# Kernel optimization log

Measured on AMD Instinct MI355X. Metric: run time of the kernel, lower is better.

The kernel has to match this reference:

```python
import jax, jax.numpy as jnp
import numpy as np

EMBED_DIM = 384

def setup_inputs() -> dict:
    key = jax.random.key(0)
    k1, k2, k3 = jax.random.split(key, 3)
    B, P, N, d = 8, 4, 4096, EMBED_DIM
    hidden_states = jax.random.normal(k1, (B, P, N, d), dtype=jnp.float32)
    # 1x1 conv == pointwise linear over channel dim; scale like fan-in init
    w_qkv = jax.random.normal(k2, (d, 1 + 2 * d), dtype=jnp.float32) * (1.0 / np.sqrt(d))
    b_qkv = jnp.zeros((1 + 2 * d,), dtype=jnp.float32)
    w_out = jax.random.normal(k3, (d, d), dtype=jnp.float32) * (1.0 / np.sqrt(d))
    b_out = jnp.zeros((d,), dtype=jnp.float32)
    return {"hidden_states": hidden_states, "w_qkv": w_qkv, "b_qkv": b_qkv,
            "w_out": w_out, "b_out": b_out}

def reference(hidden_states, w_qkv, b_qkv, w_out, b_out):
    d = EMBED_DIM
    # qkv 1x1 conv (channels-last): [B,P,N,d] @ [d, 1+2d]
    qkv = jnp.einsum("bpnd,de->bpne", hidden_states, w_qkv) + b_qkv
    query = qkv[..., :1]                # [B,P,N,1]
    key_ = qkv[..., 1:1 + d]            # [B,P,N,d]
    value = qkv[..., 1 + d:]            # [B,P,N,d]
    # softmax over token axis (axis=2); attn_dropout=0.0 -> identity
    context_scores = jax.nn.softmax(query, axis=2)
    # softmax-weighted pooling of keys over tokens -> [B,P,1,d]
    context_vector = jnp.sum(key_ * context_scores, axis=2, keepdims=True)
    # relu-gated broadcast multiply
    out = context_vector * jax.nn.relu(value)
    # out 1x1 conv
    out = jnp.einsum("bpnd,de->bpne", out, w_out) + b_out
    return out
```

## Files before the change

kernel.cpp:

```cpp
#include <hip/hip_runtime.h>

#define D     384
#define E     769
#define NTOK  4096
#define BPN   32
#define NCH   64

typedef short s16x8 __attribute__((ext_vector_type(8)));
typedef float f32x4 __attribute__((ext_vector_type(4)));
typedef float f32x2 __attribute__((ext_vector_type(2)));

__device__ __forceinline__ unsigned short f2bf(float f){
  unsigned int u = __builtin_bit_cast(unsigned int, f);
  u += 0x7FFFu + ((u >> 16) & 1u);
  return (unsigned short)(u >> 16);
}

__global__ void k0_prep(const float* __restrict__ wqkv, const float* __restrict__ wout,
                        float* __restrict__ wq, unsigned short* __restrict__ wvF,
                        unsigned short* __restrict__ woF){
  int tid = blockIdx.x*256 + threadIdx.x;
  if (tid < D) wq[tid] = wqkv[(size_t)tid*E];
  if (tid < 24*12*64*8){
    int pos = tid & 7;
    int lane = (tid >> 3) & 63;
    int kt  = (tid >> 9) % 12;
    int nt  = tid / 6144;
    int l15 = lane & 15, l4 = lane >> 4;
    int col = nt*16 + l15;
    int k   = kt*32 + l4*8 + pos;
    wvF[tid] = f2bf(wqkv[(size_t)k*E + 385 + col]);
    woF[tid] = f2bf(wout[(size_t)k*D + col]);
  }
}

__global__ __launch_bounds__(384)
void kA_fused(const float* __restrict__ H, const float* __restrict__ wq,
              float* __restrict__ partial, float* __restrict__ mArr,
              float* __restrict__ lArr){
  __shared__ float Hs[32][D];
  __shared__ float qs[32];
  const int ch = blockIdx.x, bp = blockIdx.y;
  const int t = threadIdx.x;
  const int wave = t >> 6, lane = t & 63;

  f32x2 wqr[3];
  #pragma unroll
  for (int seg=0;seg<3;++seg)
    wqr[seg] = *reinterpret_cast<const f32x2*>(wq + lane*2 + seg*128);

  float acc = 0.f, mRun = -3.4e38f, lRun = 0.f;

  for (int s = 0; s < 2; ++s){
    if (s) __syncthreads();
    const size_t base = (size_t)bp*NTOK + (size_t)ch*64 + s*32;

    f32x2 h[6][3];
    #pragma unroll
    for (int j=0;j<6;++j){
      int r = wave + j*6;
      if (r < 32){
        const float* hr = H + (base + r)*D + lane*2;
        #pragma unroll
        for (int seg=0;seg<3;++seg)
          h[j][seg] = *reinterpret_cast<const f32x2*>(hr + seg*128);
      }
    }
    #pragma unroll
    for (int j=0;j<6;++j){
      int r = wave + j*6;
      if (r < 32){
        float a = 0.f;
        #pragma unroll
        for (int seg=0;seg<3;++seg){
          *reinterpret_cast<f32x2*>(&Hs[r][lane*2 + seg*128]) = h[j][seg];
          a += h[j][seg].x*wqr[seg].x + h[j][seg].y*wqr[seg].y;
        }
        #pragma unroll
        for (int off=32; off; off>>=1) a += __shfl_xor(a, off, 64);
        if (lane == 0) qs[r] = a;
      }
    }
    __syncthreads();

    float msub = qs[0];
    #pragma unroll
    for (int n=1;n<32;++n) msub = fmaxf(msub, qs[n]);
    float mNew  = fmaxf(mRun, msub);
    float scale = __expf(mRun - mNew);
    acc  *= scale;
    lRun *= scale;
    float lsub = 0.f;
    #pragma unroll 8
    for (int n=0;n<32;++n){
      float w = __expf(qs[n] - mNew);
      lsub += w;
      acc  += w * Hs[n][t];
    }
    lRun += lsub;
    mRun  = mNew;
  }

  partial[((size_t)bp*NCH + ch)*D + t] = acc;
  if (t == 0){ mArr[bp*NCH + ch] = mRun; lArr[bp*NCH + ch] = lRun; }
}

__global__ void kB_cv(const float* __restrict__ partial, const float* __restrict__ mArr,
                      const float* __restrict__ lArr, const float* __restrict__ wqkv,
                      const float* __restrict__ bqkv, float* __restrict__ cv){
  __shared__ float S[D];
  const int bp = blockIdx.x, t = threadIdx.x;
  float M = -3.4e38f;
  #pragma unroll 4
  for (int c = 0; c < NCH; ++c) M = fmaxf(M, mArr[bp*NCH + c]);
  float num = 0.f, den = 0.f;
  #pragma unroll 2
  for (int c = 0; c < NCH; ++c){
    float f = __expf(mArr[bp*NCH + c] - M);
    num += f * partial[((size_t)bp*NCH + c)*D + t];
    den += f * lArr[bp*NCH + c];
  }
  S[t] = num / den;
  __syncthreads();
  float acc = bqkv[1 + t];
  #pragma unroll 4
  for (int k = 0; k < D; ++k)
    acc += S[k] * wqkv[(size_t)k*E + 1 + t];
  cv[(size_t)bp*D + t] = acc;
}

#define BM 64
#define LOADW(W, kt, n) (*reinterpret_cast<const s16x8*>(&(W)[((size_t)((n)*12+(kt))*64 + lane)*8]))

__global__ __launch_bounds__(512, 2)
void k5_main(const float* __restrict__ H, const unsigned short* __restrict__ wvF,
             const unsigned short* __restrict__ woF, const float* __restrict__ cv,
             const float* __restrict__ bqkv, const float* __restrict__ bout,
             float* __restrict__ out){
  __shared__ unsigned short As[BM*D];
  const int bp = blockIdx.y;
  const int m0 = blockIdx.x*BM;
  const size_t rowbase = (size_t)bp*NTOK + m0;
  const float* A = H + rowbase*D;
  const int t = threadIdx.x;
  const int wave = t>>6, lane = t&63;
  const int l15 = lane&15, l4 = lane>>4;
  const int n0 = wave*48;
  const unsigned short* wvW = wvF + (size_t)wave*3*12*512;
  const unsigned short* woW = woF + (size_t)wave*3*12*512;

  #pragma unroll
  for (int i=0;i<12;++i){
    int c = t + i*512;
    int idx8 = c >> 1;
    int l15v = idx8 & 15;
    int l4v  = (idx8 >> 4) & 3;
    int ktv  = (idx8 >> 6) % 12;
    int mv   = idx8 / 768;
    f32x4 v = *reinterpret_cast<const f32x4*>(
        A + (size_t)(mv*16 + l15v)*D + ktv*32 + l4v*8 + (c&1)*4);
    ushort4 b;
    b.x=f2bf(v.x); b.y=f2bf(v.y); b.z=f2bf(v.z); b.w=f2bf(v.w);
    *reinterpret_cast<ushort4*>(&As[c*4]) = b;
  }

  s16x8 b0[3], b1[3];
  #pragma unroll
  for (int n=0;n<3;++n) b0[n] = LOADW(wvW, 0, n);
  #pragma unroll
  for (int n=0;n<3;++n) b1[n] = LOADW(wvW, 1, n);
  __syncthreads();

  f32x4 acc[4][3] = {};
  #pragma unroll
  for (int kt=0; kt<12; ++kt){
    s16x8 bp_[3];
    if (kt < 10){
      #pragma unroll
      for (int n=0;n<3;++n) bp_[n] = LOADW(wvW, kt+2, n);
    }
    s16x8 a[4];
    #pragma unroll
    for (int m=0;m<4;++m)
      a[m] = *reinterpret_cast<const s16x8*>(&As[((m*12+kt)*64 + lane)*8]);
    #pragma unroll
    for (int m=0;m<4;++m)
      #pragma unroll
      for (int n=0;n<3;++n)
        acc[m][n] = __builtin_amdgcn_mfma_f32_16x16x32_bf16(a[m], b0[n], acc[m][n], 0,0,0);
    #pragma unroll
    for (int n=0;n<3;++n){ b0[n] = b1[n]; b1[n] = bp_[n]; }
  }
  __syncthreads();

  float bv[3], cvv[3];
  #pragma unroll
  for (int n=0;n<3;++n){
    int col = n0 + n*16 + l15;
    bv[n]  = bqkv[385+col];
    cvv[n] = cv[(size_t)bp*D + col];
  }

  #pragma unroll
  for (int n=0;n<3;++n){
    int col  = n0 + n*16 + l15;
    int kt2  = col >> 5;
    int l42  = (col >> 3) & 3;
    int pos2 = col & 7;
    #pragma unroll
    for (int m=0;m<4;++m){
      #pragma unroll
      for (int r=0;r<4;++r){
        int row = l4*4 + r;
        float v = acc[m][n][r] + bv[n];
        v = v > 0.f ? v*cvv[n] : 0.f;
        As[((m*12+kt2)*64 + l42*16 + row)*8 + pos2] = f2bf(v);
      }
    }
  }
  #pragma unroll
  for (int m=0;m<4;++m)
    #pragma unroll
    for (int n=0;n<3;++n)
      acc[m][n] = (f32x4){0.f,0.f,0.f,0.f};

  #pragma unroll
  for (int n=0;n<3;++n) b0[n] = LOADW(woW, 0, n);
  #pragma unroll
  for (int n=0;n<3;++n) b1[n] = LOADW(woW, 1, n);
  __syncthreads();

  #pragma unroll
  for (int kt=0; kt<12; ++kt){
    s16x8 bp_[3];
    if (kt < 10){
      #pragma unroll
      for (int n=0;n<3;++n) bp_[n] = LOADW(woW, kt+2, n);
    }
    s16x8 a[4];
    #pragma unroll
    for (int m=0;m<4;++m)
      a[m] = *reinterpret_cast<const s16x8*>(&As[((m*12+kt)*64 + lane)*8]);
    #pragma unroll
    for (int m=0;m<4;++m)
      #pragma unroll
      for (int n=0;n<3;++n)
        acc[m][n] = __builtin_amdgcn_mfma_f32_16x16x32_bf16(a[m], b0[n], acc[m][n], 0,0,0);
    #pragma unroll
    for (int n=0;n<3;++n){ b0[n] = b1[n]; b1[n] = bp_[n]; }
  }

  #pragma unroll
  for (int n=0;n<3;++n){
    int col = n0 + n*16 + l15;
    float bo = bout[col];
    #pragma unroll
    for (int m=0;m<4;++m)
      #pragma unroll
      for (int r=0;r<4;++r){
        int row = m*16 + l4*4 + r;
        out[(rowbase+row)*D + col] = acc[m][n][r] + bo;
      }
  }
}

extern "C" void kernel_launch(void* const* d_in, const int* in_sizes, int n_in,
                              void* d_out, int out_size, void* d_ws, size_t ws_size,
                              hipStream_t stream){
  const float* H    = (const float*)d_in[0];
  const float* wqkv = (const float*)d_in[1];
  const float* bqkv = (const float*)d_in[2];
  const float* wout = (const float*)d_in[3];
  const float* bout = (const float*)d_in[4];
  float* out = (float*)d_out;

  char* ws = (char*)d_ws;
  float*          partial = (float*)(ws + 0x000000);
  float*          mArr    = (float*)(ws + 0x300000);
  float*          lArr    = (float*)(ws + 0x302000);
  float*          cv      = (float*)(ws + 0x304000);
  float*          wq      = (float*)(ws + 0x310000);
  unsigned short* wvF     = (unsigned short*)(ws + 0x311000);
  unsigned short* woF     = (unsigned short*)(ws + 0x359000);

  hipLaunchKernelGGL(k0_prep,  dim3(576),          dim3(256), 0, stream, wqkv, wout, wq, wvF, woF);
  hipLaunchKernelGGL(kA_fused, dim3(NCH, BPN),     dim3(384), 0, stream, H, wq, partial, mArr, lArr);
  hipLaunchKernelGGL(kB_cv,    dim3(BPN),          dim3(384), 0, stream, partial, mArr, lArr, wqkv, bqkv, cv);
  hipLaunchKernelGGL(k5_main,  dim3(NTOK/BM, BPN), dim3(512), 0, stream, H, wvF, woF, cv, bqkv, bout, out);
}
```

Baseline: 227.1 us.

## Prefetch second token chunk during pooling and compute softmax weights once per block

The fused pooling kernel now issues the global loads for the second 32-token chunk before it pools the first chunk, so that memory latency overlaps with the LDS accumulation. The softmax max, exponentials and sum are computed once by wave 0 with shuffle reductions and written to shared memory. Previously every thread repeated 32 exponentials and a serial max over the chunk. This adds barriers and keeps a full chunk of H in registers, which raises register pressure.

```diff
diff --git a/kernel.cpp b/kernel.cpp
--- a/kernel.cpp
+++ b/kernel.cpp
@@ -40,6 +40,8 @@
               float* __restrict__ lArr){
   __shared__ float Hs[32][D];
   __shared__ float qs[32];
+  __shared__ float ws[32];
+  __shared__ float scaleS;
   const int ch = blockIdx.x, bp = blockIdx.y;
   const int t = threadIdx.x;
   const int wave = t >> 6, lane = t & 63;
@@ -49,56 +51,98 @@
   for (int seg=0;seg<3;++seg)
     wqr[seg] = *reinterpret_cast<const f32x2*>(wq + lane*2 + seg*128);
 
-  float acc = 0.f, mRun = -3.4e38f, lRun = 0.f;
-
-  for (int s = 0; s < 2; ++s){
-    if (s) __syncthreads();
-    const size_t base = (size_t)bp*NTOK + (size_t)ch*64 + s*32;
-
-    f32x2 h[6][3];
-    #pragma unroll
-    for (int j=0;j<6;++j){
-      int r = wave + j*6;
-      if (r < 32){
-        const float* hr = H + (base + r)*D + lane*2;
-        #pragma unroll
-        for (int seg=0;seg<3;++seg)
-          h[j][seg] = *reinterpret_cast<const f32x2*>(hr + seg*128);
-      }
-    }
-    #pragma unroll
-    for (int j=0;j<6;++j){
-      int r = wave + j*6;
-      if (r < 32){
-        float a = 0.f;
-        #pragma unroll
-        for (int seg=0;seg<3;++seg){
-          *reinterpret_cast<f32x2*>(&Hs[r][lane*2 + seg*128]) = h[j][seg];
-          a += h[j][seg].x*wqr[seg].x + h[j][seg].y*wqr[seg].y;
+  const size_t base0 = (size_t)bp*NTOK + (size_t)ch*64;
+
+  f32x2 h[6][3];
+  #pragma unroll
+  for (int j=0;j<6;++j){
+    int r = wave + j*6;
+    if (r < 32){
+      const float* hr = H + (base0 + r)*D + lane*2;
+      #pragma unroll
+      for (int seg=0;seg<3;++seg)
+        h[j][seg] = *reinterpret_cast<const f32x2*>(hr + seg*128);
+    }
+  }
+  #pragma unroll
+  for (int j=0;j<6;++j){
+    int r = wave + j*6;
+    if (r < 32){
+      float a = 0.f;
+      #pragma unroll
+      for (int seg=0;seg<3;++seg){
+        *reinterpret_cast<f32x2*>(&Hs[r][lane*2 + seg*128]) = h[j][seg];
+        a += h[j][seg].x*wqr[seg].x + h[j][seg].y*wqr[seg].y;
+      }
+      #pragma unroll
+      for (int off=32; off; off>>=1) a += __shfl_xor(a, off, 64);
+      if (lane == 0) qs[r] = a;
+    }
+  }
+  __syncthreads();
+
+  float acc = 0.f;
+  float mRun = -3.4e38f, lRun = 0.f;
+
+  #pragma unroll 1
+  for (int s=0; s<2; ++s){
+    if (s == 0){
+      #pragma unroll
+      for (int j=0;j<6;++j){
+        int r = wave + j*6;
+        if (r < 32){
+          const float* hr = H + (base0 + 32 + r)*D + lane*2;
+          #pragma unroll
+          for (int seg=0;seg<3;++seg)
+            h[j][seg] = *reinterpret_cast<const f32x2*>(hr + seg*128);
         }
-        #pragma unroll
-        for (int off=32; off; off>>=1) a += __shfl_xor(a, off, 64);
-        if (lane == 0) qs[r] = a;
-      }
+      }
+    }
+
+    if (wave == 0){
+      float q = (lane < 32) ? qs[lane] : -3.4e38f;
+      float msub = q;
+      #pragma unroll
+      for (int off=32; off; off>>=1) msub = fmaxf(msub, __shfl_xor(msub, off, 64));
+      float mNew = fmaxf(mRun, msub);
+      float sc   = __expf(mRun - mNew);
+      float e    = (lane < 32) ? __expf(q - mNew) : 0.f;
+      if (lane < 32) ws[lane] = e;
+      float lsub = e;
+      #pragma unroll
+      for (int off=32; off; off>>=1) lsub += __shfl_xor(lsub, off, 64);
+      lRun = lRun*sc + lsub;
+      mRun = mNew;
+      if (lane == 0) scaleS = sc;
     }
     __syncthreads();
 
-    float msub = qs[0];
-    #pragma unroll
-    for (int n=1;n<32;++n) msub = fmaxf(msub, qs[n]);
-    float mNew  = fmaxf(mRun, msub);
-    float scale = __expf(mRun - mNew);
-    acc  *= scale;
-    lRun *= scale;
-    float lsub = 0.f;
+    float sc = scaleS;
+    float a2 = 0.f;
     #pragma unroll 8
-    for (int n=0;n<32;++n){
-      float w = __expf(qs[n] - mNew);
-      lsub += w;
-      acc  += w * Hs[n][t];
-    }
-    lRun += lsub;
-    mRun  = mNew;
+    for (int n=0;n<32;++n)
+      a2 += ws[n] * Hs[n][t];
+    acc = acc*sc + a2;
+    __syncthreads();
+
+    if (s == 0){
+      #pragma unroll
+      for (int j=0;j<6;++j){
+        int r = wave + j*6;
+        if (r < 32){
+          float a = 0.f;
+          #pragma unroll
+          for (int seg=0;seg<3;++seg){
+            *reinterpret_cast<f32x2*>(&Hs[r][lane*2 + seg*128]) = h[j][seg];
+            a += h[j][seg].x*wqr[seg].x + h[j][seg].y*wqr[seg].y;
+          }
+          #pragma unroll
+          for (int off=32; off; off>>=1) a += __shfl_xor(a, off, 64);
+          if (lane == 0) qs[r] = a;
+        }
+      }
+      __syncthreads();
+    }
   }
 
   partial[((size_t)bp*NCH + ch)*D + t] = acc;
```

Measured after the change: 225.6 us. No clear change (-0.6%).

## Drop LDS staging in query pooling; reread H chunk from cache after one-shot softmax

Applied to the files above, without the earlier changes.

The fused query/pooling kernel no longer stages 32-row tiles of H in shared memory with an online-softmax rescale across two sub-chunks. It now computes all 64 query scores first, does one max/exp/sum per chunk with wave-level shuffles, and then reads the 64x384 chunk of H a second time from global memory (expected to hit in cache) for the weighted sum. This frees about 48KB of LDS per block, which should allow more resident blocks, and removes the rescale arithmetic. The cost is a second pass over H that relies on L2 or LLC residency and could add global traffic.

```diff
diff --git a/kernel.cpp b/kernel.cpp
--- a/kernel.cpp
+++ b/kernel.cpp
@@ -38,71 +38,62 @@
 void kA_fused(const float* __restrict__ H, const float* __restrict__ wq,
               float* __restrict__ partial, float* __restrict__ mArr,
               float* __restrict__ lArr){
-  __shared__ float Hs[32][D];
-  __shared__ float qs[32];
+  __shared__ float qs[64];
+  __shared__ float ws[64];
   const int ch = blockIdx.x, bp = blockIdx.y;
   const int t = threadIdx.x;
   const int wave = t >> 6, lane = t & 63;
+  const size_t base = (size_t)bp*NTOK + (size_t)ch*64;
 
   f32x2 wqr[3];
   #pragma unroll
   for (int seg=0;seg<3;++seg)
     wqr[seg] = *reinterpret_cast<const f32x2*>(wq + lane*2 + seg*128);
 
-  float acc = 0.f, mRun = -3.4e38f, lRun = 0.f;
-
-  for (int s = 0; s < 2; ++s){
-    if (s) __syncthreads();
-    const size_t base = (size_t)bp*NTOK + (size_t)ch*64 + s*32;
-
-    f32x2 h[6][3];
-    #pragma unroll
-    for (int j=0;j<6;++j){
-      int r = wave + j*6;
-      if (r < 32){
-        const float* hr = H + (base + r)*D + lane*2;
-        #pragma unroll
-        for (int seg=0;seg<3;++seg)
-          h[j][seg] = *reinterpret_cast<const f32x2*>(hr + seg*128);
-      }
-    }
-    #pragma unroll
-    for (int j=0;j<6;++j){
-      int r = wave + j*6;
-      if (r < 32){
-        float a = 0.f;
-        #pragma unroll
-        for (int seg=0;seg<3;++seg){
-          *reinterpret_cast<f32x2*>(&Hs[r][lane*2 + seg*128]) = h[j][seg];
-          a += h[j][seg].x*wqr[seg].x + h[j][seg].y*wqr[seg].y;
-        }
-        #pragma unroll
-        for (int off=32; off; off>>=1) a += __shfl_xor(a, off, 64);
-        if (lane == 0) qs[r] = a;
-      }
-    }
-    __syncthreads();
-
-    float msub = qs[0];
-    #pragma unroll
-    for (int n=1;n<32;++n) msub = fmaxf(msub, qs[n]);
-    float mNew  = fmaxf(mRun, msub);
-    float scale = __expf(mRun - mNew);
-    acc  *= scale;
-    lRun *= scale;
-    float lsub = 0.f;
-    #pragma unroll 8
-    for (int n=0;n<32;++n){
-      float w = __expf(qs[n] - mNew);
-      lsub += w;
-      acc  += w * Hs[n][t];
-    }
-    lRun += lsub;
-    mRun  = mNew;
-  }
-
+  #pragma unroll
+  for (int j=0;j<11;++j){
+    int r = wave + j*6;
+    if (r < 64){
+      const float* hr = H + (base + r)*D + lane*2;
+      f32x2 h0 = *reinterpret_cast<const f32x2*>(hr);
+      f32x2 h1 = *reinterpret_cast<const f32x2*>(hr + 128);
+      f32x2 h2 = *reinterpret_cast<const f32x2*>(hr + 256);
+      float a = h0.x*wqr[0].x + h0.y*wqr[0].y
+              + h1.x*wqr[1].x + h1.y*wqr[1].y
+              + h2.x*wqr[2].x + h2.y*wqr[2].y;
+      #pragma unroll
+      for (int off=32; off; off>>=1) a += __shfl_xor(a, off, 64);
+      if (lane == 0) qs[r] = a;
+    }
+  }
+  __syncthreads();
+
+  if (wave == 0){
+    float q = qs[lane];
+    float m = q;
+    #pragma unroll
+    for (int off=32; off; off>>=1) m = fmaxf(m, __shfl_xor(m, off, 64));
+    float e = __expf(q - m);
+    ws[lane] = e;
+    float l = e;
+    #pragma unroll
+    for (int off=32; off; off>>=1) l += __shfl_xor(l, off, 64);
+    if (lane == 0){ mArr[bp*NCH + ch] = m; lArr[bp*NCH + ch] = l; }
+  }
+  __syncthreads();
+
+  float acc = 0.f;
+  #pragma unroll
+  for (int nb=0; nb<8; ++nb){
+    float hv[8];
+    #pragma unroll
+    for (int i=0;i<8;++i)
+      hv[i] = H[(base + nb*8 + i)*D + t];
+    #pragma unroll
+    for (int i=0;i<8;++i)
+      acc += ws[nb*8+i] * hv[i];
+  }
   partial[((size_t)bp*NCH + ch)*D + t] = acc;
-  if (t == 0){ mArr[bp*NCH + ch] = mRun; lArr[bp*NCH + ch] = lRun; }
 }
 
 __global__ void kB_cv(const float* __restrict__ partial, const float* __restrict__ mArr,
```

Result: slower. 244.8 us (+7.8%).
